# Optimization experiments

Measured on AMD Instinct MI355X. Metric: run time of the kernel, lower is better.

The kernel has to match this reference:

```python
import jax, jax.numpy as jnp
import numpy as np
from jax import lax

PROB_THRESHOLD = 0.9
IOU_THRESHOLD = 0.5
H, W = 80, 80


def setup_inputs() -> dict:
    key = jax.random.key(0)
    # [5, H, W]: channel 0 = probability, channels 1:5 = (x1, y1, w, h)
    x = jax.random.uniform(key, (5, H, W), dtype=jnp.float32)
    return {"x": x}


def _pairwise_iou(boxes):
    # boxes: [N, 4] in xyxy format (torchvision box_iou semantics, no +1)
    area = jnp.maximum(boxes[:, 2] - boxes[:, 0], 0.0) * jnp.maximum(boxes[:, 3] - boxes[:, 1], 0.0)
    lt = jnp.maximum(boxes[:, None, :2], boxes[None, :, :2])  # [N, N, 2]
    rb = jnp.minimum(boxes[:, None, 2:], boxes[None, :, 2:])  # [N, N, 2]
    wh = jnp.maximum(rb - lt, 0.0)
    inter = wh[..., 0] * wh[..., 1]                           # [N, N]
    union = area[:, None] + area[None, :] - inter
    return inter / jnp.maximum(union, 1e-9)


def reference(x):
    # Flatten grid: rows = [prob, x1, y1, w, h]
    flat = x.reshape(5, -1).T  # [N, 5]
    valid = flat[:, 0] > PROB_THRESHOLD

    # Faithful in-place transform from the torch code:
    #   bbx[:, 2] = bbx[:, 0] + bbx[:, 2];  bbx[:, 3] = bbx[:, 1] + bbx[:, 3]
    # (column 0 is the probability channel, exactly as the source does it)
    c2 = flat[:, 0] + flat[:, 2]
    c3 = flat[:, 1] + flat[:, 3]
    b5 = jnp.stack([flat[:, 0], flat[:, 1], c2, c3, flat[:, 4]], axis=1)  # [N, 5]

    # Sort by score descending; invalid rows pushed to the end with -inf
    scores = jnp.where(valid, b5[:, 0], -jnp.inf)
    order = jnp.argsort(-scores)
    b5_sorted = b5[order]          # [N, 5]
    valid_sorted = valid[order]    # [N]
    boxes = b5_sorted[:, 1:]       # [N, 4] -> nms(boxes=x[:,1:], scores=x[:,0])

    iou = _pairwise_iou(boxes)     # [N, N], dominant 164 MB intermediate
    N = boxes.shape[0]

    # Greedy NMS in score order: keep box i iff it is valid and no already-kept
    # higher-scoring box overlaps it with IoU > threshold.
    def body(i, keep):
        suppressed = jnp.any(keep & (iou[i] > IOU_THRESHOLD))
        return keep.at[i].set(valid_sorted[i] & ~suppressed)

    keep = lax.fori_loop(0, N, body, jnp.zeros((N,), dtype=bool))

    # Fixed-shape, jit-friendly equivalent of x[bbxis]: kept rows (score-sorted),
    # suppressed / below-threshold rows zeroed out.
    return jnp.where(keep[:, None], b5_sorted, 0.0)
```

## Files before the change

### kernel.cpp

```cpp
#include <hip/hip_runtime.h>


#define NTH   1024
#define MAXV  2048
#define MAXM  256

__global__ __launch_bounds__(NTH, 1) void nms_all(
    const float* __restrict__ X, float* __restrict__ out, int n, int out_n) {
  __shared__ __align__(16) float cscore[MAXV];
  __shared__ unsigned int cidx[MAXV];
  __shared__ int s_vcount, s_mcount, sflag;
  __shared__ int   prank[MAXM];
  __shared__ float pbox[MAXM][4];
  __shared__ float parea[MAXM];
  __shared__ int   srank[MAXM];
  __shared__ float sbox[MAXM][4];
  __shared__ float sarea[MAXM];
  __shared__ int   skeep[MAXM];
  const int t = threadIdx.x;
  if (t == 0) { s_vcount = 0; s_mcount = 0; }

  const float4* X4 = (const float4*)X;
  const int n4 = n >> 2;
  float4 sc0 = make_float4(-1.f, -1.f, -1.f, -1.f);
  float4 sc1 = sc0;
  if (t < n4)        sc0 = X4[t];
  if (t + NTH < n4)  sc1 = X4[t + NTH];

  float4* out4 = (float4*)out;
  const int o4 = out_n >> 2;
  for (int i = t; i < o4; i += NTH)
    out4[i] = make_float4(0.f, 0.f, 0.f, 0.f);
  for (int i = (o4 << 2) + t; i < out_n; i += NTH) out[i] = 0.f;

  __syncthreads();

  if (t < n4) {
    float v[4] = {sc0.x, sc0.y, sc0.z, sc0.w};
    #pragma unroll
    for (int k = 0; k < 4; ++k)
      if (v[k] > 0.9f) {
        int p = atomicAdd(&s_vcount, 1);
        if (p < MAXV) { cscore[p] = v[k]; cidx[p] = (unsigned)(4 * t + k); }
      }
  }
  if (t + NTH < n4) {
    float v[4] = {sc1.x, sc1.y, sc1.z, sc1.w};
    #pragma unroll
    for (int k = 0; k < 4; ++k)
      if (v[k] > 0.9f) {
        int p = atomicAdd(&s_vcount, 1);
        if (p < MAXV) { cscore[p] = v[k]; cidx[p] = (unsigned)(4 * (t + NTH) + k); }
      }
  }
  for (int i = (n4 << 2) + t; i < n; i += NTH) {
    float s = X[i];
    if (s > 0.9f) {
      int p = atomicAdd(&s_vcount, 1);
      if (p < MAXV) { cscore[p] = s; cidx[p] = (unsigned)i; }
    }
  }
  __syncthreads();

  const int V = min(s_vcount, MAXV);
  const int V4 = (V + 3) & ~3;
  for (int e = V + t; e < V4; e += NTH) cscore[e] = -1.f;
  __syncthreads();

  const float4* c4 = (const float4*)cscore;
  const int nq = V4 >> 2;
  for (int e = t; e < V; e += NTH) {
    float s = cscore[e];
    unsigned idx = cidx[e];
    int gt = 0, eq = 0;
    for (int q = 0; q < nq; ++q) {
      float4 v = c4[q];
      gt += (v.x > s) + (v.y > s) + (v.z > s) + (v.w > s);
      eq += (v.x == s) + (v.y == s) + (v.z == s) + (v.w == s);
    }
    eq -= 1;
    int rank = gt;
    if (eq > 0) {
      int lt = 0;
      for (int m = 0; m < V; ++m)
        lt += (cscore[m] == s) && (cidx[m] < idx);
      rank += lt;
    }
    float f1 = X[n + idx], f2 = X[2 * n + idx];
    float f3 = X[3 * n + idx], f4v = X[4 * n + idx];
    float c2 = s + f2, c3 = f1 + f3;
    float* row = out + (size_t)rank * 5;
    row[0] = s; row[1] = f1; row[2] = c2; row[3] = c3; row[4] = f4v;
    float w = fmaxf(c3 - f1, 0.f);
    float h = fmaxf(f4v - c2, 0.f);
    float area = w * h;
    if (area > 0.f) {
      int p = atomicAdd(&s_mcount, 1);
      if (p < MAXM) {
        prank[p] = rank;
        pbox[p][0] = f1; pbox[p][1] = c2; pbox[p][2] = c3; pbox[p][3] = f4v;
        parea[p] = area;
      }
    }
  }
  __syncthreads();

  const int M = min(s_mcount, MAXM);
  for (int e = t; e < M; e += NTH) {
    int r = prank[e];
    int pos = 0;
    for (int m = 0; m < M; ++m) pos += (prank[m] < r);
    srank[pos] = r;
    sbox[pos][0] = pbox[e][0]; sbox[pos][1] = pbox[e][1];
    sbox[pos][2] = pbox[e][2]; sbox[pos][3] = pbox[e][3];
    sarea[pos] = parea[e];
    skeep[pos] = 1;
  }
  __syncthreads();

  for (int i = 1; i < M; ++i) {
    if (t == 0) sflag = 0;
    __syncthreads();
    if (t < i && skeep[t]) {
      float ltx = fmaxf(sbox[t][0], sbox[i][0]);
      float lty = fmaxf(sbox[t][1], sbox[i][1]);
      float rbx = fminf(sbox[t][2], sbox[i][2]);
      float rby = fminf(sbox[t][3], sbox[i][3]);
      float w = fmaxf(rbx - ltx, 0.f);
      float h = fmaxf(rby - lty, 0.f);
      float inter = w * h;
      float uni = sarea[t] + sarea[i] - inter;
      if (inter / fmaxf(uni, 1e-9f) > 0.5f) sflag = 1;
    }
    __syncthreads();
    if (t == 0 && sflag) skeep[i] = 0;
    __syncthreads();
  }

  for (int e = t; e < M; e += NTH) {
    if (!skeep[e]) {
      float* row = out + (size_t)srank[e] * 5;
      row[0] = 0.f; row[1] = 0.f; row[2] = 0.f; row[3] = 0.f; row[4] = 0.f;
    }
  }
}

extern "C" void kernel_launch(void* const* d_in, const int* in_sizes, int n_in,
                              void* d_out, int out_size, void* d_ws, size_t ws_size,
                              hipStream_t stream) {
  const float* X = (const float*)d_in[0];
  float* out = (float*)d_out;
  int n = in_sizes[0] / 5;
  (void)d_ws; (void)ws_size;
  hipLaunchKernelGGL(nms_all, dim3(1), dim3(NTH), 0, stream, X, out, n, out_size);
}
```

Baseline: 71.01 us.

## Split compaction into multi-block kernel before single-block rank and NMS

Adds a 32-block pre-pass that zeroes the output, filters scores above threshold, and gathers the box fields plus area into per-block records in workspace. A second single-block kernel concatenates these records, ranks two candidates per thread, and runs the same greedy NMS. The aim is to spread the global-memory gathers and output zeroing across many CUs instead of one block. The cost is a second launch and a workspace round-trip, and the original single-kernel path stays as a fallback when workspace is too small.

```diff
diff --git a/kernel.cpp b/kernel.cpp
--- a/kernel.cpp
+++ b/kernel.cpp
@@ -1,11 +1,216 @@
 #include <hip/hip_runtime.h>
 
 
-#define NTH   1024
+#define K1B   32
+#define K1T   256
+#define CAP   256
 #define MAXV  2048
 #define MAXM  256
-
-__global__ __launch_bounds__(NTH, 1) void nms_all(
+#define NTH   1024
+
+__global__ __launch_bounds__(K1T) void k_compact(
+    const float* __restrict__ X, float* __restrict__ out,
+    float* __restrict__ recs, int* __restrict__ counts, int n, int out_n) {
+  __shared__ int lcnt;
+  const int b = blockIdx.x, t = threadIdx.x;
+  if (t == 0) lcnt = 0;
+  __syncthreads();
+
+  const int gid = b * K1T + t;
+  float4* out4 = (float4*)out;
+  const int o4 = out_n >> 2;
+  for (int i = gid; i < o4; i += K1B * K1T)
+    out4[i] = make_float4(0.f, 0.f, 0.f, 0.f);
+  for (int i = (o4 << 2) + gid; i < out_n; i += K1B * K1T) out[i] = 0.f;
+
+  const int n4 = n >> 2;
+  const int sl = (n4 + K1B - 1) / K1B;
+  const int q0 = b * sl, q1 = min(q0 + sl, n4);
+  const float4* X4 = (const float4*)X;
+  float* myrec = recs + (size_t)b * CAP * 8;
+  for (int q = q0 + t; q < q1; q += K1T) {
+    float4 v = X4[q];
+    float vv[4] = {v.x, v.y, v.z, v.w};
+    #pragma unroll
+    for (int k = 0; k < 4; ++k) {
+      float s = vv[k];
+      if (s > 0.9f) {
+        int idx = 4 * q + k;
+        int p = atomicAdd(&lcnt, 1);
+        if (p < CAP) {
+          float f1 = X[n + idx], f2 = X[2 * n + idx];
+          float f3 = X[3 * n + idx], f4v = X[4 * n + idx];
+          float c2 = s + f2, c3 = f1 + f3;
+          float w = fmaxf(c3 - f1, 0.f);
+          float h = fmaxf(f4v - c2, 0.f);
+          float area = w * h;
+          float4* e = (float4*)(myrec + (size_t)p * 8);
+          e[0] = make_float4(s, f1, c2, c3);
+          e[1] = make_float4(f4v, area, __int_as_float(idx), 0.f);
+        }
+      }
+    }
+  }
+  if (b == 0) {
+    for (int i = (n4 << 2) + t; i < n; i += K1T) {
+      float s = X[i];
+      if (s > 0.9f) {
+        int p = atomicAdd(&lcnt, 1);
+        if (p < CAP) {
+          float f1 = X[n + i], f2 = X[2 * n + i];
+          float f3 = X[3 * n + i], f4v = X[4 * n + i];
+          float c2 = s + f2, c3 = f1 + f3;
+          float w = fmaxf(c3 - f1, 0.f);
+          float h = fmaxf(f4v - c2, 0.f);
+          float area = w * h;
+          float4* e = (float4*)(myrec + (size_t)p * 8);
+          e[0] = make_float4(s, f1, c2, c3);
+          e[1] = make_float4(f4v, area, __int_as_float(i), 0.f);
+        }
+      }
+    }
+  }
+  __syncthreads();
+  if (t == 0) counts[b] = min(lcnt, CAP);
+}
+
+__global__ __launch_bounds__(NTH, 1) void k_rank_nms(
+    const float* __restrict__ recs, const int* __restrict__ counts,
+    float* __restrict__ out) {
+  __shared__ int scnt[K1B];
+  __shared__ int soff[K1B + 1];
+  __shared__ __align__(16) float srec[MAXV][8];
+  __shared__ __align__(16) float cscore[MAXV];
+  __shared__ unsigned cidx[MAXV];
+  __shared__ int s_m, sflag;
+  __shared__ int   prank[MAXM];
+  __shared__ float pbox[MAXM][4];
+  __shared__ float parea[MAXM];
+  __shared__ int   srnk[MAXM];
+  __shared__ float sbox[MAXM][4];
+  __shared__ float sarea[MAXM];
+  __shared__ int   skeep[MAXM];
+  const int t = threadIdx.x;
+  if (t == 0) s_m = 0;
+  if (t < K1B) scnt[t] = counts[t];
+  __syncthreads();
+  if (t == 0) {
+    int acc = 0;
+    for (int b = 0; b < K1B; ++b) { soff[b] = acc; acc += scnt[b]; }
+    soff[K1B] = acc;
+  }
+  __syncthreads();
+  const int V = min(soff[K1B], MAXV);
+
+  for (int d = t; d < V; d += NTH) {
+    int lo = 0, hi = K1B;
+    while (hi - lo > 1) { int mid = (lo + hi) >> 1; if (soff[mid] <= d) lo = mid; else hi = mid; }
+    int i = d - soff[lo];
+    const float4* src = (const float4*)(recs + ((size_t)lo * CAP + i) * 8);
+    float4 r0 = src[0], r1 = src[1];
+    ((float4*)srec[d])[0] = r0;
+    ((float4*)srec[d])[1] = r1;
+    cscore[d] = r0.x;
+    cidx[d]   = __float_as_uint(r1.z);
+  }
+  const int V4 = (V + 3) & ~3;
+  for (int e = V + t; e < V4; e += NTH) cscore[e] = -1.f;
+  __syncthreads();
+
+  const float4* c4 = (const float4*)cscore;
+  const int nq = V4 >> 2;
+  const int e0 = 2 * t, e1 = 2 * t + 1;
+  const bool a0 = (e0 < V), a1 = (e1 < V);
+  float s0 = a0 ? cscore[e0] : 0.f;
+  float s1 = a1 ? cscore[e1] : 0.f;
+  int gt0 = 0, eq0 = 0, gt1 = 0, eq1 = 0;
+  if (a0) {
+    for (int q = 0; q < nq; ++q) {
+      float4 v = c4[q];
+      gt0 += (v.x > s0) + (v.y > s0) + (v.z > s0) + (v.w > s0);
+      eq0 += (v.x == s0) + (v.y == s0) + (v.z == s0) + (v.w == s0);
+      gt1 += (v.x > s1) + (v.y > s1) + (v.z > s1) + (v.w > s1);
+      eq1 += (v.x == s1) + (v.y == s1) + (v.z == s1) + (v.w == s1);
+    }
+  }
+  int rank0 = gt0, rank1 = gt1;
+  if (a0 && eq0 - 1 > 0) {
+    unsigned idx = cidx[e0];
+    int lt = 0;
+    for (int m = 0; m < V; ++m) lt += (cscore[m] == s0) && (cidx[m] < idx);
+    rank0 = gt0 + lt;
+  }
+  if (a1 && eq1 - 1 > 0) {
+    unsigned idx = cidx[e1];
+    int lt = 0;
+    for (int m = 0; m < V; ++m) lt += (cscore[m] == s1) && (cidx[m] < idx);
+    rank1 = gt1 + lt;
+  }
+
+  #pragma unroll
+  for (int h = 0; h < 2; ++h) {
+    const bool act = h ? a1 : a0;
+    if (!act) continue;
+    const int e = h ? e1 : e0;
+    const int r = h ? rank1 : rank0;
+    float* row = out + (size_t)r * 5;
+    row[0] = srec[e][0]; row[1] = srec[e][1]; row[2] = srec[e][2];
+    row[3] = srec[e][3]; row[4] = srec[e][4];
+    float area = srec[e][5];
+    if (area > 0.f) {
+      int p = atomicAdd(&s_m, 1);
+      if (p < MAXM) {
+        prank[p] = r;
+        pbox[p][0] = srec[e][1]; pbox[p][1] = srec[e][2];
+        pbox[p][2] = srec[e][3]; pbox[p][3] = srec[e][4];
+        parea[p] = area;
+      }
+    }
+  }
+  __syncthreads();
+
+  const int M = min(s_m, MAXM);
+  for (int e = t; e < M; e += NTH) {
+    int r = prank[e];
+    int pos = 0;
+    for (int m = 0; m < M; ++m) pos += (prank[m] < r);
+    srnk[pos] = r;
+    sbox[pos][0] = pbox[e][0]; sbox[pos][1] = pbox[e][1];
+    sbox[pos][2] = pbox[e][2]; sbox[pos][3] = pbox[e][3];
+    sarea[pos] = parea[e];
+    skeep[pos] = 1;
+  }
+  __syncthreads();
+
+  for (int i = 1; i < M; ++i) {
+    if (t == 0) sflag = 0;
+    __syncthreads();
+    if (t < i && skeep[t]) {
+      float ltx = fmaxf(sbox[t][0], sbox[i][0]);
+      float lty = fmaxf(sbox[t][1], sbox[i][1]);
+      float rbx = fminf(sbox[t][2], sbox[i][2]);
+      float rby = fminf(sbox[t][3], sbox[i][3]);
+      float w = fmaxf(rbx - ltx, 0.f);
+      float h = fmaxf(rby - lty, 0.f);
+      float inter = w * h;
+      float uni = sarea[t] + sarea[i] - inter;
+      if (inter / fmaxf(uni, 1e-9f) > 0.5f) sflag = 1;
+    }
+    __syncthreads();
+    if (t == 0 && sflag) skeep[i] = 0;
+    __syncthreads();
+  }
+
+  for (int e = t; e < M; e += NTH) {
+    if (!skeep[e]) {
+      float* row = out + (size_t)srnk[e] * 5;
+      row[0] = 0.f; row[1] = 0.f; row[2] = 0.f; row[3] = 0.f; row[4] = 0.f;
+    }
+  }
+}
+
+#define FB_NTH 1024
+__global__ __launch_bounds__(FB_NTH, 1) void nms_all(
     const float* __restrict__ X, float* __restrict__ out, int n, int out_n) {
   __shared__ __align__(16) float cscore[MAXV];
   __shared__ unsigned int cidx[MAXV];
@@ -13,28 +218,23 @@
   __shared__ int   prank[MAXM];
   __shared__ float pbox[MAXM][4];
   __shared__ float parea[MAXM];
-  __shared__ int   srank[MAXM];
+  __shared__ int   srnk[MAXM];
   __shared__ float sbox[MAXM][4];
   __shared__ float sarea[MAXM];
   __shared__ int   skeep[MAXM];
   const int t = threadIdx.x;
   if (t == 0) { s_vcount = 0; s_mcount = 0; }
-
   const float4* X4 = (const float4*)X;
   const int n4 = n >> 2;
   float4 sc0 = make_float4(-1.f, -1.f, -1.f, -1.f);
   float4 sc1 = sc0;
-  if (t < n4)        sc0 = X4[t];
-  if (t + NTH < n4)  sc1 = X4[t + NTH];
-
+  if (t < n4)           sc0 = X4[t];
+  if (t + FB_NTH < n4)  sc1 = X4[t + FB_NTH];
   float4* out4 = (float4*)out;
   const int o4 = out_n >> 2;
-  for (int i = t; i < o4; i += NTH)
-    out4[i] = make_float4(0.f, 0.f, 0.f, 0.f);
-  for (int i = (o4 << 2) + t; i < out_n; i += NTH) out[i] = 0.f;
-
-  __syncthreads();
-
+  for (int i = t; i < o4; i += FB_NTH) out4[i] = make_float4(0.f, 0.f, 0.f, 0.f);
+  for (int i = (o4 << 2) + t; i < out_n; i += FB_NTH) out[i] = 0.f;
+  __syncthreads();
   if (t < n4) {
     float v[4] = {sc0.x, sc0.y, sc0.z, sc0.w};
     #pragma unroll
@@ -44,16 +244,16 @@
         if (p < MAXV) { cscore[p] = v[k]; cidx[p] = (unsigned)(4 * t + k); }
       }
   }
-  if (t + NTH < n4) {
+  if (t + FB_NTH < n4) {
     float v[4] = {sc1.x, sc1.y, sc1.z, sc1.w};
     #pragma unroll
     for (int k = 0; k < 4; ++k)
       if (v[k] > 0.9f) {
         int p = atomicAdd(&s_vcount, 1);
-        if (p < MAXV) { cscore[p] = v[k]; cidx[p] = (unsigned)(4 * (t + NTH) + k); }
-      }
-  }
-  for (int i = (n4 << 2) + t; i < n; i += NTH) {
+        if (p < MAXV) { cscore[p] = v[k]; cidx[p] = (unsigned)(4 * (t + FB_NTH) + k); }
+      }
+  }
+  for (int i = (n4 << 2) + t; i < n; i += FB_NTH) {
     float s = X[i];
     if (s > 0.9f) {
       int p = atomicAdd(&s_vcount, 1);
@@ -61,15 +261,13 @@
     }
   }
   __syncthreads();
-
   const int V = min(s_vcount, MAXV);
   const int V4 = (V + 3) & ~3;
-  for (int e = V + t; e < V4; e += NTH) cscore[e] = -1.f;
-  __syncthreads();
-
+  for (int e = V + t; e < V4; e += FB_NTH) cscore[e] = -1.f;
+  __syncthreads();
   const float4* c4 = (const float4*)cscore;
   const int nq = V4 >> 2;
-  for (int e = t; e < V; e += NTH) {
+  for (int e = t; e < V; e += FB_NTH) {
     float s = cscore[e];
     unsigned idx = cidx[e];
     int gt = 0, eq = 0;
@@ -82,8 +280,7 @@
     int rank = gt;
     if (eq > 0) {
       int lt = 0;
-      for (int m = 0; m < V; ++m)
-        lt += (cscore[m] == s) && (cidx[m] < idx);
+      for (int m = 0; m < V; ++m) lt += (cscore[m] == s) && (cidx[m] < idx);
       rank += lt;
     }
     float f1 = X[n + idx], f2 = X[2 * n + idx];
@@ -104,20 +301,18 @@
     }
   }
   __syncthreads();
-
   const int M = min(s_mcount, MAXM);
-  for (int e = t; e < M; e += NTH) {
+  for (int e = t; e < M; e += FB_NTH) {
     int r = prank[e];
     int pos = 0;
     for (int m = 0; m < M; ++m) pos += (prank[m] < r);
-    srank[pos] = r;
+    srnk[pos] = r;
     sbox[pos][0] = pbox[e][0]; sbox[pos][1] = pbox[e][1];
     sbox[pos][2] = pbox[e][2]; sbox[pos][3] = pbox[e][3];
     sarea[pos] = parea[e];
     skeep[pos] = 1;
   }
   __syncthreads();
-
   for (int i = 1; i < M; ++i) {
     if (t == 0) sflag = 0;
     __syncthreads();
@@ -136,10 +331,9 @@
     if (t == 0 && sflag) skeep[i] = 0;
     __syncthreads();
   }
-
-  for (int e = t; e < M; e += NTH) {
+  for (int e = t; e < M; e += FB_NTH) {
     if (!skeep[e]) {
-      float* row = out + (size_t)srank[e] * 5;
+      float* row = out + (size_t)srnk[e] * 5;
       row[0] = 0.f; row[1] = 0.f; row[2] = 0.f; row[3] = 0.f; row[4] = 0.f;
     }
   }
@@ -151,6 +345,15 @@
   const float* X = (const float*)d_in[0];
   float* out = (float*)d_out;
   int n = in_sizes[0] / 5;
-  (void)d_ws; (void)ws_size;
-  hipLaunchKernelGGL(nms_all, dim3(1), dim3(NTH), 0, stream, X, out, n, out_size);
+  size_t need = 256 + (size_t)K1B * CAP * 8 * sizeof(float);
+  if (ws_size >= need) {
+    int* counts = (int*)d_ws;
+    float* recs = (float*)((char*)d_ws + 256);
+    hipLaunchKernelGGL(k_compact, dim3(K1B), dim3(K1T), 0, stream,
+                       X, out, recs, counts, n, out_size);
+    hipLaunchKernelGGL(k_rank_nms, dim3(1), dim3(NTH), 0, stream,
+                       recs, counts, out);
+  } else {
+    hipLaunchKernelGGL(nms_all, dim3(1), dim3(FB_NTH), 0, stream, X, out, n, out_size);
+  }
 }
```

Result: slower. 78.36 us (+10.4%).

## Split NMS into multi-block rank/scatter kernel plus single-block suppression kernel

Applied to the files above, without the earlier changes.

Replaces the single-block kernel with a grid of blocks. Each block computes global ranks for 64 candidates by splitting the comparison against all scores across 16 wavefronts, writes output rows directly (zeros for invalid rows), and appends positive-area boxes to per-block workspace lists. A second single-block kernel gathers those lists, sorts them by rank and runs the greedy suppression. This spreads the rank computation over many CUs and drops the separate output zeroing pass, at the cost of a second launch and O(n^2) global reads of scores. The old fused kernel remains as a fallback when the workspace is too small.

```diff
diff --git a/kernel.cpp b/kernel.cpp
--- a/kernel.cpp
+++ b/kernel.cpp
@@ -1,11 +1,162 @@
 #include <hip/hip_runtime.h>
 
 
-#define NTH   1024
-#define MAXV  2048
+#define BT    1024
+#define NCH   16
+#define CPB   64
+#define CAPB  64
 #define MAXM  256
-
-__global__ __launch_bounds__(NTH, 1) void nms_all(
+#define K2T   256
+
+__global__ __launch_bounds__(BT) void k_main(
+    const float* __restrict__ X, float* __restrict__ out,
+    float* __restrict__ lists, int* __restrict__ counts, int n) {
+  __shared__ unsigned pp[CPB][NCH];
+  __shared__ int lcnt;
+  const int b = blockIdx.x;
+  const int t = threadIdx.x;
+  const int w = t >> 6;
+  const int l = t & 63;
+  const int c = b * CPB + l;
+  const int n4 = n >> 2;
+  const int CQ = (n4 + NCH - 1) / NCH;
+  if (t == 0) lcnt = 0;
+
+  float si = (c < n) ? X[c] : -1.f;
+
+  const float4* X4 = (const float4*)X;
+  const int q0 = w * CQ, q1 = min(q0 + CQ, n4);
+  int gt = 0, eq = 0;
+  for (int q = q0; q < q1; ++q) {
+    float4 v = X4[q];
+    gt += (v.x > si) + (v.y > si) + (v.z > si) + (v.w > si);
+    eq += (v.x == si) + (v.y == si) + (v.z == si) + (v.w == si);
+  }
+  if (w == NCH - 1) {
+    for (int j = n4 << 2; j < n; ++j) {
+      float sj = X[j];
+      gt += (sj > si); eq += (sj == si);
+    }
+  }
+  pp[l][w] = (unsigned)gt | ((unsigned)eq << 16);
+  __syncthreads();
+
+  if (w == 0 && c < n) {
+    int gts = 0, eqs = 0;
+    for (int k = 0; k < NCH; ++k) {
+      unsigned p = pp[l][k];
+      gts += (int)(p & 0xffffu);
+      eqs += (int)(p >> 16);
+    }
+    eqs -= 1;
+    int pos = gts;
+    if (eqs > 0) {
+      const int kc = min(c / (4 * CQ), NCH - 1);
+      int lte = 0;
+      for (int k = 0; k < kc; ++k) lte += (int)(pp[l][k] >> 16);
+      const int start = 4 * kc * CQ;
+      for (int j = start; j < c; ++j) lte += (X[j] == si);
+      pos += lte;
+    }
+    float* row = out + (size_t)pos * 5;
+    if (si > 0.9f) {
+      float f1 = X[n + c], f2 = X[2 * n + c];
+      float f3 = X[3 * n + c], f4v = X[4 * n + c];
+      float c2 = si + f2, c3 = f1 + f3;
+      row[0] = si; row[1] = f1; row[2] = c2; row[3] = c3; row[4] = f4v;
+      float bw = fmaxf(c3 - f1, 0.f);
+      float bh = fmaxf(f4v - c2, 0.f);
+      float area = bw * bh;
+      if (area > 0.f) {
+        int p = atomicAdd(&lcnt, 1);
+        if (p < CAPB) {
+          float4* e = (float4*)(lists + ((size_t)b * CAPB + p) * 8);
+          e[0] = make_float4(__int_as_float(pos), f1, c2, c3);
+          e[1] = make_float4(f4v, area, 0.f, 0.f);
+        }
+      }
+    } else {
+      row[0] = 0.f; row[1] = 0.f; row[2] = 0.f; row[3] = 0.f; row[4] = 0.f;
+    }
+    if (l == 0) counts[b] = lcnt;
+  }
+}
+
+__global__ __launch_bounds__(K2T) void k_nms(
+    const float* __restrict__ lists, const int* __restrict__ counts,
+    float* __restrict__ out, int nb) {
+  __shared__ int s_m, sflag;
+  __shared__ int   prank[MAXM];
+  __shared__ float pbox[MAXM][4];
+  __shared__ float parea[MAXM];
+  __shared__ int   srnk[MAXM];
+  __shared__ float sbox[MAXM][4];
+  __shared__ float sarea[MAXM];
+  __shared__ int   skeep[MAXM];
+  const int t = threadIdx.x;
+  if (t == 0) s_m = 0;
+  __syncthreads();
+
+  for (int b = t; b < nb; b += K2T) {
+    int cb = counts[b];
+    if (cb > CAPB) cb = CAPB;
+    for (int e = 0; e < cb; ++e) {
+      const float4* src = (const float4*)(lists + ((size_t)b * CAPB + e) * 8);
+      float4 r0 = src[0], r1 = src[1];
+      int p = atomicAdd(&s_m, 1);
+      if (p < MAXM) {
+        prank[p] = __float_as_int(r0.x);
+        pbox[p][0] = r0.y; pbox[p][1] = r0.z; pbox[p][2] = r0.w;
+        pbox[p][3] = r1.x;
+        parea[p] = r1.y;
+      }
+    }
+  }
+  __syncthreads();
+  const int M = min(s_m, MAXM);
+
+  for (int e = t; e < M; e += K2T) {
+    int r = prank[e];
+    int pos = 0;
+    for (int m = 0; m < M; ++m) pos += (prank[m] < r);
+    srnk[pos] = r;
+    sbox[pos][0] = pbox[e][0]; sbox[pos][1] = pbox[e][1];
+    sbox[pos][2] = pbox[e][2]; sbox[pos][3] = pbox[e][3];
+    sarea[pos] = parea[e];
+    skeep[pos] = 1;
+  }
+  __syncthreads();
+
+  for (int i = 1; i < M; ++i) {
+    if (t == 0) sflag = 0;
+    __syncthreads();
+    if (t < i && skeep[t]) {
+      float ltx = fmaxf(sbox[t][0], sbox[i][0]);
+      float lty = fmaxf(sbox[t][1], sbox[i][1]);
+      float rbx = fminf(sbox[t][2], sbox[i][2]);
+      float rby = fminf(sbox[t][3], sbox[i][3]);
+      float w = fmaxf(rbx - ltx, 0.f);
+      float h = fmaxf(rby - lty, 0.f);
+      float inter = w * h;
+      float uni = sarea[t] + sarea[i] - inter;
+      if (inter / fmaxf(uni, 1e-9f) > 0.5f) sflag = 1;
+    }
+    __syncthreads();
+    if (t == 0 && sflag) skeep[i] = 0;
+    __syncthreads();
+  }
+
+  for (int e = t; e < M; e += K2T) {
+    if (!skeep[e]) {
+      float* row = out + (size_t)srnk[e] * 5;
+      row[0] = 0.f; row[1] = 0.f; row[2] = 0.f; row[3] = 0.f; row[4] = 0.f;
+    }
+  }
+}
+
+#define FB_NTH 1024
+#define MAXV   2048
+__global__ __launch_bounds__(FB_NTH, 1) void nms_all(
     const float* __restrict__ X, float* __restrict__ out, int n, int out_n) {
   __shared__ __align__(16) float cscore[MAXV];
   __shared__ unsigned int cidx[MAXV];
@@ -13,28 +164,23 @@
   __shared__ int   prank[MAXM];
   __shared__ float pbox[MAXM][4];
   __shared__ float parea[MAXM];
-  __shared__ int   srank[MAXM];
+  __shared__ int   srnk[MAXM];
   __shared__ float sbox[MAXM][4];
   __shared__ float sarea[MAXM];
   __shared__ int   skeep[MAXM];
   const int t = threadIdx.x;
   if (t == 0) { s_vcount = 0; s_mcount = 0; }
-
   const float4* X4 = (const float4*)X;
   const int n4 = n >> 2;
   float4 sc0 = make_float4(-1.f, -1.f, -1.f, -1.f);
   float4 sc1 = sc0;
-  if (t < n4)        sc0 = X4[t];
-  if (t + NTH < n4)  sc1 = X4[t + NTH];
-
+  if (t < n4)           sc0 = X4[t];
+  if (t + FB_NTH < n4)  sc1 = X4[t + FB_NTH];
   float4* out4 = (float4*)out;
   const int o4 = out_n >> 2;
-  for (int i = t; i < o4; i += NTH)
-    out4[i] = make_float4(0.f, 0.f, 0.f, 0.f);
-  for (int i = (o4 << 2) + t; i < out_n; i += NTH) out[i] = 0.f;
-
-  __syncthreads();
-
+  for (int i = t; i < o4; i += FB_NTH) out4[i] = make_float4(0.f, 0.f, 0.f, 0.f);
+  for (int i = (o4 << 2) + t; i < out_n; i += FB_NTH) out[i] = 0.f;
+  __syncthreads();
   if (t < n4) {
     float v[4] = {sc0.x, sc0.y, sc0.z, sc0.w};
     #pragma unroll
@@ -44,16 +190,16 @@
         if (p < MAXV) { cscore[p] = v[k]; cidx[p] = (unsigned)(4 * t + k); }
       }
   }
-  if (t + NTH < n4) {
+  if (t + FB_NTH < n4) {
     float v[4] = {sc1.x, sc1.y, sc1.z, sc1.w};
     #pragma unroll
     for (int k = 0; k < 4; ++k)
       if (v[k] > 0.9f) {
         int p = atomicAdd(&s_vcount, 1);
-        if (p < MAXV) { cscore[p] = v[k]; cidx[p] = (unsigned)(4 * (t + NTH) + k); }
-      }
-  }
-  for (int i = (n4 << 2) + t; i < n; i += NTH) {
+        if (p < MAXV) { cscore[p] = v[k]; cidx[p] = (unsigned)(4 * (t + FB_NTH) + k); }
+      }
+  }
+  for (int i = (n4 << 2) + t; i < n; i += FB_NTH) {
     float s = X[i];
     if (s > 0.9f) {
       int p = atomicAdd(&s_vcount, 1);
@@ -61,15 +207,13 @@
     }
   }
   __syncthreads();
-
   const int V = min(s_vcount, MAXV);
   const int V4 = (V + 3) & ~3;
-  for (int e = V + t; e < V4; e += NTH) cscore[e] = -1.f;
-  __syncthreads();
-
+  for (int e = V + t; e < V4; e += FB_NTH) cscore[e] = -1.f;
+  __syncthreads();
   const float4* c4 = (const float4*)cscore;
   const int nq = V4 >> 2;
-  for (int e = t; e < V; e += NTH) {
+  for (int e = t; e < V; e += FB_NTH) {
     float s = cscore[e];
     unsigned idx = cidx[e];
     int gt = 0, eq = 0;
@@ -82,8 +226,7 @@
     int rank = gt;
     if (eq > 0) {
       int lt = 0;
-      for (int m = 0; m < V; ++m)
-        lt += (cscore[m] == s) && (cidx[m] < idx);
+      for (int m = 0; m < V; ++m) lt += (cscore[m] == s) && (cidx[m] < idx);
       rank += lt;
     }
     float f1 = X[n + idx], f2 = X[2 * n + idx];
@@ -104,20 +247,18 @@
     }
   }
   __syncthreads();
-
   const int M = min(s_mcount, MAXM);
-  for (int e = t; e < M; e += NTH) {
+  for (int e = t; e < M; e += FB_NTH) {
     int r = prank[e];
     int pos = 0;
     for (int m = 0; m < M; ++m) pos += (prank[m] < r);
-    srank[pos] = r;
+    srnk[pos] = r;
     sbox[pos][0] = pbox[e][0]; sbox[pos][1] = pbox[e][1];
     sbox[pos][2] = pbox[e][2]; sbox[pos][3] = pbox[e][3];
     sarea[pos] = parea[e];
     skeep[pos] = 1;
   }
   __syncthreads();
-
   for (int i = 1; i < M; ++i) {
     if (t == 0) sflag = 0;
     __syncthreads();
@@ -136,10 +277,9 @@
     if (t == 0 && sflag) skeep[i] = 0;
     __syncthreads();
   }
-
-  for (int e = t; e < M; e += NTH) {
+  for (int e = t; e < M; e += FB_NTH) {
     if (!skeep[e]) {
-      float* row = out + (size_t)srank[e] * 5;
+      float* row = out + (size_t)srnk[e] * 5;
       row[0] = 0.f; row[1] = 0.f; row[2] = 0.f; row[3] = 0.f; row[4] = 0.f;
     }
   }
@@ -151,6 +291,17 @@
   const float* X = (const float*)d_in[0];
   float* out = (float*)d_out;
   int n = in_sizes[0] / 5;
-  (void)d_ws; (void)ws_size;
-  hipLaunchKernelGGL(nms_all, dim3(1), dim3(NTH), 0, stream, X, out, n, out_size);
+  int nb = (n + CPB - 1) / CPB;
+  size_t need = 1024 + (size_t)nb * CAPB * 8 * sizeof(float);
+  if (ws_size >= need) {
+    int* counts = (int*)d_ws;
+    float* lists = (float*)((char*)d_ws + 1024);
+    hipLaunchKernelGGL(k_main, dim3(nb), dim3(BT), 0, stream,
+                       X, out, lists, counts, n);
+    hipLaunchKernelGGL(k_nms, dim3(1), dim3(K2T), 0, stream,
+                       lists, counts, out, nb);
+  } else {
+    hipLaunchKernelGGL(nms_all, dim3(1), dim3(FB_NTH), 0, stream,
+                       X, out, n, out_size);
+  }
 }
```

Result: slower. 86.55 us (+21.9%).
